# Optimization experiments

Hardware: AMD Instinct MI355X
Metric: run time of the kernel (lower is better)

The kernel has to match this reference:

```python
import jax, jax.numpy as jnp
import numpy as np

B, S, H = 2, 256, 256
R = H  # rdim defaults to hidden_size


def setup_inputs() -> dict:
    key = jax.random.key(0)
    k1, k2, k3 = jax.random.split(key, 3)
    hidden_states = jax.random.normal(k1, (B, S, H), dtype=jnp.float32)
    # Linear weights stored torch-style [out, in]
    Wqkv = jax.random.normal(k2, (3 * R, H), dtype=jnp.float32) * (H ** -0.5)
    bqkv = jnp.zeros((3 * R,), dtype=jnp.float32)
    Wc = jax.random.normal(k3, (R, R), dtype=jnp.float32) * (R ** -0.5)
    bc = jnp.zeros((R,), dtype=jnp.float32)
    return {"hidden_states": hidden_states, "Wqkv": Wqkv, "bqkv": bqkv, "Wc": Wc, "bc": bc}


def reference(hidden_states, Wqkv, bqkv, Wc, bc):
    # qkv projection: [B,S,3R]
    qkv = jnp.einsum('bsh,rh->bsr', hidden_states, Wqkv) + bqkv
    q, k, v = jnp.split(qkv, 3, axis=-1)  # each [B,S,R]
    # Tucker-style outer-product scores: [B,S,L,R]
    scores = jnp.einsum('bsr,blr->bslr', q, k)
    # c_proj mixes the r dimension
    scores = jnp.einsum('bslr,pr->bslp', scores, Wc) + bc
    # rearrange 'b s l r -> (b r) s l' + softmax(dim=-1) == softmax over l axis
    probs = jax.nn.softmax(scores, axis=2)
    # 'brsl,blr->bsr' after rearrange back == 'bslr,blr->bsr'
    return jnp.einsum('bslr,blr->bsr', probs, v)
```

## Files before the change

### kernel.cpp

```cpp
#include <hip/hip_runtime.h>
#include <hip/hip_bf16.h>
#include <math.h>

typedef __bf16 bf16;
typedef _Float16 f16;
typedef __attribute__((ext_vector_type(8))) __bf16 bf16x8;
typedef __attribute__((ext_vector_type(8))) _Float16 f16x8;
typedef __attribute__((ext_vector_type(4))) _Float16 f16x4;
typedef __attribute__((ext_vector_type(4))) float floatx4;

__device__ __forceinline__ void split8(floatx4 a0, floatx4 a1, bf16x8& hi, bf16x8& lo) {
#pragma unroll
    for (int t = 0; t < 4; t++) {
        float v0 = a0[t], v1 = a1[t];
        bf16 h0 = (bf16)v0, h1 = (bf16)v1;
        hi[t] = h0;     lo[t] = (bf16)(v0 - (float)h0);
        hi[t + 4] = h1; lo[t + 4] = (bf16)(v1 - (float)h1);
    }
}

__global__ __launch_bounds__(256, 4)
void proj_kernel(const float* __restrict__ hs, const float* __restrict__ Wq,
                 const float* __restrict__ bq, const float* __restrict__ Wc,
                 f16* __restrict__ q_ws, f16* __restrict__ k_ws,
                 f16* __restrict__ vT_ws, f16* __restrict__ Wc_ws)
{
    const int tid = threadIdx.x;
    if (blockIdx.x >= 384) {
        const int base = (blockIdx.x - 384) * 1024 + tid * 4;
        floatx4 w = *(const floatx4*)(Wc + base);
        f16x4 h;
        h.x = (f16)w.x; h.y = (f16)w.y; h.z = (f16)w.z; h.w = (f16)w.w;
        *(f16x4*)(Wc_ws + base) = h;
        return;
    }
    const int wv = tid >> 6, lane = tid & 63;
    const int quad = lane >> 4, lcol = lane & 15;
    const int wt = blockIdx.x * 4 + wv;
    const int rt = wt / 48, ct = wt - rt * 48;
    const int row0 = rt * 16, col0 = ct * 16;

    const float* arow = hs + (row0 + lcol) * 256;
    const float* brow = Wq + (col0 + lcol) * 256;

    floatx4 acc = {0.f, 0.f, 0.f, 0.f};
#pragma unroll
    for (int ks = 0; ks < 8; ks++) {
        const int h = ks * 32 + quad * 8;
        floatx4 a0 = *(const floatx4*)(arow + h);
        floatx4 a1 = *(const floatx4*)(arow + h + 4);
        floatx4 b0 = *(const floatx4*)(brow + h);
        floatx4 b1 = *(const floatx4*)(brow + h + 4);
        bf16x8 ahi, alo, bhi, blo;
        split8(a0, a1, ahi, alo);
        split8(b0, b1, bhi, blo);
        acc = __builtin_amdgcn_mfma_f32_16x16x32_bf16(ahi, bhi, acc, 0, 0, 0);
        acc = __builtin_amdgcn_mfma_f32_16x16x32_bf16(ahi, blo, acc, 0, 0, 0);
        acc = __builtin_amdgcn_mfma_f32_16x16x32_bf16(alo, bhi, acc, 0, 0, 0);
    }
    const float bias = bq[col0 + lcol];
    const int col = col0 + lcol, seg = col0 >> 8, jj = col & 255;
#pragma unroll
    for (int r = 0; r < 4; r++) {
        const int row = row0 + quad * 4 + r;
        const float val = acc[r] + bias;
        if (seg == 0)      q_ws[row * 256 + jj] = (f16)val;
        else if (seg == 1) k_ws[row * 256 + jj] = (f16)val;
        else               vT_ws[(row >> 8) * 65536 + jj * 256 + (row & 255)] = (f16)val;
    }
}

__global__ __launch_bounds__(512, 2)
void attn_main(const f16* __restrict__ qw, const f16* __restrict__ kw,
               const f16* __restrict__ vT, const f16* __restrict__ Wc16,
               float* __restrict__ out)
{
    __shared__ f16 Wlds[64 * 256];
    __shared__ float obuf[4][4][64];
    __shared__ float sbuf[4][4][64];

    const int bid = blockIdx.x;
    const int pt = bid & 3;
    const int sg = (bid >> 2) & 63;
    const int b  = bid >> 8;
    const int p0 = pt * 64;
    const int tid  = threadIdx.x;
    const int wv   = tid >> 6;
    const int lane = tid & 63;
    const int quad = lane >> 4, lcol = lane & 15;
    const int lq = wv & 3, sh = wv >> 2;
    const int l0w = lq * 64;

    const f16* kbase = kw + b * 65536;
    const f16* vbase = vT + b * 65536;

#pragma unroll
    for (int it = 0; it < 4; it++) {
        const int id = tid + it * 512;
        const int r = id >> 5, c = id & 31;
        const int csrc = c ^ (r & 7);
        uint4 d = *(const uint4*)(Wc16 + (p0 + r) * 256 + csrc * 8);
        *(uint4*)(Wlds + r * 256 + c * 8) = d;
    }
    __syncthreads();

    float osum[2][4], ssum[2][4];

#pragma unroll
    for (int sl = 0; sl < 2; sl++) {
        const int s = sg * 4 + sh * 2 + sl;
        const f16* qrow = qw + (b * 256 + s) * 256;

        floatx4 acc[4][4];
#pragma unroll
        for (int i = 0; i < 4; i++)
#pragma unroll
            for (int j = 0; j < 4; j++)
                acc[i][j] = (floatx4){0.f, 0.f, 0.f, 0.f};

#pragma unroll
        for (int kk = 0; kk < 8; kk++) {
            const int rb = kk * 32 + quad * 8;
            f16x8 qv = *(const f16x8*)(qrow + rb);
            f16x8 kf[4];
#pragma unroll
            for (int i = 0; i < 4; i++)
                kf[i] = *(const f16x8*)(kbase + (l0w + i * 16 + lcol) * 256 + rb);
#pragma unroll
            for (int j = 0; j < 4; j++) {
                f16x8 w8 = *(const f16x8*)(Wlds + (j * 16 + lcol) * 256 +
                                           (((kk * 4 + quad) ^ (lcol & 7)) << 3));
                f16x8 bfr = w8 * qv;
#pragma unroll
                for (int i = 0; i < 4; i++)
                    acc[i][j] = __builtin_amdgcn_mfma_f32_16x16x32_f16(kf[i], bfr, acc[i][j], 0, 0, 0);
            }
        }

        float os[4] = {0.f, 0.f, 0.f, 0.f}, ss[4] = {0.f, 0.f, 0.f, 0.f};
#pragma unroll
        for (int i = 0; i < 4; i++) {
#pragma unroll
            for (int j = 0; j < 4; j++) {
                f16x4 vf = *(const f16x4*)(vbase + (p0 + j * 16 + lcol) * 256 + l0w + i * 16 + quad * 4);
#pragma unroll
                for (int t = 0; t < 4; t++) {
                    const float P = __expf(acc[i][j][t]);
                    os[j] = fmaf(P, (float)vf[t], os[j]);
                    ss[j] += P;
                }
            }
        }
#pragma unroll
        for (int j = 0; j < 4; j++) {
            os[j] += __shfl_xor(os[j], 16);
            os[j] += __shfl_xor(os[j], 32);
            ss[j] += __shfl_xor(ss[j], 16);
            ss[j] += __shfl_xor(ss[j], 32);
            osum[sl][j] = os[j];
            ssum[sl][j] = ss[j];
        }
    }

    if (quad == 0) {
#pragma unroll
        for (int sl = 0; sl < 2; sl++)
#pragma unroll
            for (int j = 0; j < 4; j++) {
                obuf[lq][sh * 2 + sl][j * 16 + lcol] = osum[sl][j];
                sbuf[lq][sh * 2 + sl][j * 16 + lcol] = ssum[sl][j];
            }
    }
    __syncthreads();

    if (tid < 256) {
        const int slot = tid >> 6, p = tid & 63;
        const float O = obuf[0][slot][p] + obuf[1][slot][p] + obuf[2][slot][p] + obuf[3][slot][p];
        const float S = sbuf[0][slot][p] + sbuf[1][slot][p] + sbuf[2][slot][p] + sbuf[3][slot][p];
        out[(b * 256 + sg * 4 + slot) * 256 + p0 + p] = O / S;
    }
}

extern "C" void kernel_launch(void* const* d_in, const int* in_sizes, int n_in,
                              void* d_out, int out_size, void* d_ws, size_t ws_size,
                              hipStream_t stream) {
    const float* hs   = (const float*)d_in[0];
    const float* Wqkv = (const float*)d_in[1];
    const float* bqkv = (const float*)d_in[2];
    const float* Wc   = (const float*)d_in[3];
    float* out = (float*)d_out;

    char* ws = (char*)d_ws;
    f16* q_ws   = (f16*)ws;
    f16* k_ws   = (f16*)(ws + 262144);
    f16* vT_ws  = (f16*)(ws + 524288);
    f16* Wc_ws  = (f16*)(ws + 786432);

    proj_kernel<<<dim3(448), 256, 0, stream>>>(hs, Wqkv, bqkv, Wc, q_ws, k_ws, vT_ws, Wc_ws);
    attn_main<<<dim3(512), 512, 0, stream>>>(q_ws, k_ws, vT_ws, Wc_ws, out);
}
```

Measured before the change: 101.2 us.

## Stage K tiles through LDS with register prefetch, remap waves to seq/l-halves

Each wave now owns one query row and half of a 64-wide l tile. K is staged in 64-row chunks through a swizzled LDS buffer, and the next chunk is prefetched into registers while the current one is consumed. Before, each wave read K fragments straight from global memory, so this shares K across waves through LDS and shrinks the cross-wave reduction to two partials. The cost is extra LDS (32KB more), block-wide barriers in every l-chunk iteration, and a serialized four-step loop.

```diff
diff --git a/kernel.cpp b/kernel.cpp
--- a/kernel.cpp
+++ b/kernel.cpp
@@ -76,8 +76,9 @@
                float* __restrict__ out)
 {
     __shared__ f16 Wlds[64 * 256];
-    __shared__ float obuf[4][4][64];
-    __shared__ float sbuf[4][4][64];
+    __shared__ f16 Klds[64 * 256];
+    __shared__ float obuf[2][4][64];
+    __shared__ float sbuf[2][4][64];
 
     const int bid = blockIdx.x;
     const int pt = bid & 3;
@@ -88,32 +89,52 @@
     const int wv   = tid >> 6;
     const int lane = tid & 63;
     const int quad = lane >> 4, lcol = lane & 15;
-    const int lq = wv & 3, sh = wv >> 2;
-    const int l0w = lq * 64;
+    const int sslot = wv & 3, lh = wv >> 2;
+    const int s = sg * 4 + sslot;
 
     const f16* kbase = kw + b * 65536;
     const f16* vbase = vT + b * 65536;
+    const f16* qrow  = qw + (b * 256 + s) * 256;
 
 #pragma unroll
     for (int it = 0; it < 4; it++) {
-        const int id = tid + it * 512;
+        const int id = it * 512 + tid;
         const int r = id >> 5, c = id & 31;
         const int csrc = c ^ (r & 7);
-        uint4 d = *(const uint4*)(Wc16 + (p0 + r) * 256 + csrc * 8);
-        *(uint4*)(Wlds + r * 256 + c * 8) = d;
-    }
-    __syncthreads();
-
-    float osum[2][4], ssum[2][4];
-
-#pragma unroll
-    for (int sl = 0; sl < 2; sl++) {
-        const int s = sg * 4 + sh * 2 + sl;
-        const f16* qrow = qw + (b * 256 + s) * 256;
-
-        floatx4 acc[4][4];
-#pragma unroll
-        for (int i = 0; i < 4; i++)
+        *(uint4*)(Wlds + r * 256 + c * 8) =
+            *(const uint4*)(Wc16 + (p0 + r) * 256 + csrc * 8);
+    }
+
+    uint4 st[4];
+#pragma unroll
+    for (int it = 0; it < 4; it++) {
+        const int id = it * 512 + tid;
+        const int r = id >> 5, csrc = (id & 31) ^ (r & 7);
+        st[it] = *(const uint4*)(kbase + r * 256 + csrc * 8);
+    }
+
+    float os[4] = {0.f, 0.f, 0.f, 0.f}, ss[4] = {0.f, 0.f, 0.f, 0.f};
+
+    for (int lq = 0; lq < 4; lq++) {
+#pragma unroll
+        for (int it = 0; it < 4; it++) {
+            const int id = it * 512 + tid;
+            const int r = id >> 5, c = id & 31;
+            *(uint4*)(Klds + r * 256 + c * 8) = st[it];
+        }
+        if (lq < 3) {
+#pragma unroll
+            for (int it = 0; it < 4; it++) {
+                const int id = it * 512 + tid;
+                const int r = id >> 5, csrc = (id & 31) ^ (r & 7);
+                st[it] = *(const uint4*)(kbase + ((lq + 1) * 64 + r) * 256 + csrc * 8);
+            }
+        }
+        __syncthreads();
+
+        floatx4 acc[2][4];
+#pragma unroll
+        for (int i = 0; i < 2; i++)
 #pragma unroll
             for (int j = 0; j < 4; j++)
                 acc[i][j] = (floatx4){0.f, 0.f, 0.f, 0.f};
@@ -122,27 +143,24 @@
         for (int kk = 0; kk < 8; kk++) {
             const int rb = kk * 32 + quad * 8;
             f16x8 qv = *(const f16x8*)(qrow + rb);
-            f16x8 kf[4];
-#pragma unroll
-            for (int i = 0; i < 4; i++)
-                kf[i] = *(const f16x8*)(kbase + (l0w + i * 16 + lcol) * 256 + rb);
+            const int sw = ((kk * 4 + quad) ^ (lcol & 7)) << 3;
+            f16x8 kf0 = *(const f16x8*)(Klds + (lh * 32 + lcol) * 256 + sw);
+            f16x8 kf1 = *(const f16x8*)(Klds + (lh * 32 + 16 + lcol) * 256 + sw);
 #pragma unroll
             for (int j = 0; j < 4; j++) {
-                f16x8 w8 = *(const f16x8*)(Wlds + (j * 16 + lcol) * 256 +
-                                           (((kk * 4 + quad) ^ (lcol & 7)) << 3));
+                f16x8 w8 = *(const f16x8*)(Wlds + (j * 16 + lcol) * 256 + sw);
                 f16x8 bfr = w8 * qv;
-#pragma unroll
-                for (int i = 0; i < 4; i++)
-                    acc[i][j] = __builtin_amdgcn_mfma_f32_16x16x32_f16(kf[i], bfr, acc[i][j], 0, 0, 0);
+                acc[0][j] = __builtin_amdgcn_mfma_f32_16x16x32_f16(kf0, bfr, acc[0][j], 0, 0, 0);
+                acc[1][j] = __builtin_amdgcn_mfma_f32_16x16x32_f16(kf1, bfr, acc[1][j], 0, 0, 0);
             }
         }
 
-        float os[4] = {0.f, 0.f, 0.f, 0.f}, ss[4] = {0.f, 0.f, 0.f, 0.f};
-#pragma unroll
-        for (int i = 0; i < 4; i++) {
+        const int lbase = lq * 64 + lh * 32;
+#pragma unroll
+        for (int i = 0; i < 2; i++) {
 #pragma unroll
             for (int j = 0; j < 4; j++) {
-                f16x4 vf = *(const f16x4*)(vbase + (p0 + j * 16 + lcol) * 256 + l0w + i * 16 + quad * 4);
+                f16x4 vf = *(const f16x4*)(vbase + (p0 + j * 16 + lcol) * 256 + lbase + i * 16 + quad * 4);
 #pragma unroll
                 for (int t = 0; t < 4; t++) {
                     const float P = __expf(acc[i][j][t]);
@@ -151,32 +169,29 @@
                 }
             }
         }
+        if (lq < 3) __syncthreads();
+    }
+
+#pragma unroll
+    for (int j = 0; j < 4; j++) {
+        os[j] += __shfl_xor(os[j], 16);
+        os[j] += __shfl_xor(os[j], 32);
+        ss[j] += __shfl_xor(ss[j], 16);
+        ss[j] += __shfl_xor(ss[j], 32);
+    }
+    if (quad == 0) {
 #pragma unroll
         for (int j = 0; j < 4; j++) {
-            os[j] += __shfl_xor(os[j], 16);
-            os[j] += __shfl_xor(os[j], 32);
-            ss[j] += __shfl_xor(ss[j], 16);
-            ss[j] += __shfl_xor(ss[j], 32);
-            osum[sl][j] = os[j];
-            ssum[sl][j] = ss[j];
-        }
-    }
-
-    if (quad == 0) {
-#pragma unroll
-        for (int sl = 0; sl < 2; sl++)
-#pragma unroll
-            for (int j = 0; j < 4; j++) {
-                obuf[lq][sh * 2 + sl][j * 16 + lcol] = osum[sl][j];
-                sbuf[lq][sh * 2 + sl][j * 16 + lcol] = ssum[sl][j];
-            }
+            obuf[lh][sslot][j * 16 + lcol] = os[j];
+            sbuf[lh][sslot][j * 16 + lcol] = ss[j];
+        }
     }
     __syncthreads();
 
     if (tid < 256) {
         const int slot = tid >> 6, p = tid & 63;
-        const float O = obuf[0][slot][p] + obuf[1][slot][p] + obuf[2][slot][p] + obuf[3][slot][p];
-        const float S = sbuf[0][slot][p] + sbuf[1][slot][p] + sbuf[2][slot][p] + sbuf[3][slot][p];
+        const float O = obuf[0][slot][p] + obuf[1][slot][p];
+        const float S = sbuf[0][slot][p] + sbuf[1][slot][p];
         out[(b * 256 + sg * 4 + slot) * 256 + p0 + p] = O / S;
     }
 }
```

New measurement: 113.1 us. 11.7% more time.

## Split L across 8 waves and process two s rows per block

Applied to the files above, without the earlier changes.

Each block now handles 2 sequence rows instead of 4, with all 8 waves splitting the L dimension into 32-wide slices. Each wave handles both s rows, so each K fragment and Wc LDS read feeds two q rows. The grid doubles to 1024 blocks. This costs twice as many Wc tile loads into LDS across the grid and an 8-way cross-wave reduction, in exchange for better fragment reuse and more parallelism.

```diff
diff --git a/kernel.cpp b/kernel.cpp
--- a/kernel.cpp
+++ b/kernel.cpp
@@ -76,108 +76,116 @@
                float* __restrict__ out)
 {
     __shared__ f16 Wlds[64 * 256];
-    __shared__ float obuf[4][4][64];
-    __shared__ float sbuf[4][4][64];
+    __shared__ float obuf[8][2][64];
+    __shared__ float sbuf[8][2][64];
 
     const int bid = blockIdx.x;
     const int pt = bid & 3;
-    const int sg = (bid >> 2) & 63;
-    const int b  = bid >> 8;
+    const int sg = (bid >> 2) & 127;
+    const int b  = bid >> 9;
     const int p0 = pt * 64;
     const int tid  = threadIdx.x;
     const int wv   = tid >> 6;
     const int lane = tid & 63;
     const int quad = lane >> 4, lcol = lane & 15;
-    const int lq = wv & 3, sh = wv >> 2;
-    const int l0w = lq * 64;
+    const int l0w = wv * 32;
 
     const f16* kbase = kw + b * 65536;
     const f16* vbase = vT + b * 65536;
+    const f16* qrow0 = qw + (b * 256 + sg * 2) * 256;
+    const f16* qrow1 = qrow0 + 256;
 
 #pragma unroll
     for (int it = 0; it < 4; it++) {
-        const int id = tid + it * 512;
+        const int id = it * 512 + tid;
         const int r = id >> 5, c = id & 31;
         const int csrc = c ^ (r & 7);
-        uint4 d = *(const uint4*)(Wc16 + (p0 + r) * 256 + csrc * 8);
-        *(uint4*)(Wlds + r * 256 + c * 8) = d;
+        *(uint4*)(Wlds + r * 256 + c * 8) =
+            *(const uint4*)(Wc16 + (p0 + r) * 256 + csrc * 8);
     }
     __syncthreads();
 
-    float osum[2][4], ssum[2][4];
-
-#pragma unroll
-    for (int sl = 0; sl < 2; sl++) {
-        const int s = sg * 4 + sh * 2 + sl;
-        const f16* qrow = qw + (b * 256 + s) * 256;
-
-        floatx4 acc[4][4];
-#pragma unroll
-        for (int i = 0; i < 4; i++)
+    floatx4 acc[2][2][4];
+#pragma unroll
+    for (int s = 0; s < 2; s++)
+#pragma unroll
+        for (int i = 0; i < 2; i++)
 #pragma unroll
             for (int j = 0; j < 4; j++)
-                acc[i][j] = (floatx4){0.f, 0.f, 0.f, 0.f};
-
-#pragma unroll
-        for (int kk = 0; kk < 8; kk++) {
-            const int rb = kk * 32 + quad * 8;
-            f16x8 qv = *(const f16x8*)(qrow + rb);
-            f16x8 kf[4];
-#pragma unroll
-            for (int i = 0; i < 4; i++)
-                kf[i] = *(const f16x8*)(kbase + (l0w + i * 16 + lcol) * 256 + rb);
+                acc[s][i][j] = (floatx4){0.f, 0.f, 0.f, 0.f};
+
+#pragma unroll
+    for (int kk = 0; kk < 8; kk++) {
+        const int rb = kk * 32 + quad * 8;
+        f16x8 qv0 = *(const f16x8*)(qrow0 + rb);
+        f16x8 qv1 = *(const f16x8*)(qrow1 + rb);
+        f16x8 kf0 = *(const f16x8*)(kbase + (l0w + lcol) * 256 + rb);
+        f16x8 kf1 = *(const f16x8*)(kbase + (l0w + 16 + lcol) * 256 + rb);
+        const int sw = ((kk * 4 + quad) ^ (lcol & 7)) << 3;
+#pragma unroll
+        for (int j = 0; j < 4; j++) {
+            f16x8 w8 = *(const f16x8*)(Wlds + (j * 16 + lcol) * 256 + sw);
+            f16x8 bf0 = w8 * qv0;
+            f16x8 bf1 = w8 * qv1;
+            acc[0][0][j] = __builtin_amdgcn_mfma_f32_16x16x32_f16(kf0, bf0, acc[0][0][j], 0, 0, 0);
+            acc[0][1][j] = __builtin_amdgcn_mfma_f32_16x16x32_f16(kf1, bf0, acc[0][1][j], 0, 0, 0);
+            acc[1][0][j] = __builtin_amdgcn_mfma_f32_16x16x32_f16(kf0, bf1, acc[1][0][j], 0, 0, 0);
+            acc[1][1][j] = __builtin_amdgcn_mfma_f32_16x16x32_f16(kf1, bf1, acc[1][1][j], 0, 0, 0);
+        }
+    }
+
+    float os[2][4] = {{0.f,0.f,0.f,0.f},{0.f,0.f,0.f,0.f}};
+    float ss[2][4] = {{0.f,0.f,0.f,0.f},{0.f,0.f,0.f,0.f}};
+#pragma unroll
+    for (int i = 0; i < 2; i++) {
+#pragma unroll
+        for (int j = 0; j < 4; j++) {
+            f16x4 vf = *(const f16x4*)(vbase + (p0 + j * 16 + lcol) * 256 + l0w + i * 16 + quad * 4);
+            float vF0 = (float)vf[0], vF1 = (float)vf[1], vF2 = (float)vf[2], vF3 = (float)vf[3];
+#pragma unroll
+            for (int s = 0; s < 2; s++) {
+                const float P0 = __expf(acc[s][i][j][0]);
+                const float P1 = __expf(acc[s][i][j][1]);
+                const float P2 = __expf(acc[s][i][j][2]);
+                const float P3 = __expf(acc[s][i][j][3]);
+                os[s][j] = fmaf(P0, vF0, os[s][j]);
+                os[s][j] = fmaf(P1, vF1, os[s][j]);
+                os[s][j] = fmaf(P2, vF2, os[s][j]);
+                os[s][j] = fmaf(P3, vF3, os[s][j]);
+                ss[s][j] += (P0 + P1) + (P2 + P3);
+            }
+        }
+    }
+
+#pragma unroll
+    for (int s = 0; s < 2; s++)
+#pragma unroll
+        for (int j = 0; j < 4; j++) {
+            os[s][j] += __shfl_xor(os[s][j], 16);
+            os[s][j] += __shfl_xor(os[s][j], 32);
+            ss[s][j] += __shfl_xor(ss[s][j], 16);
+            ss[s][j] += __shfl_xor(ss[s][j], 32);
+        }
+    if (quad == 0) {
+#pragma unroll
+        for (int s = 0; s < 2; s++)
 #pragma unroll
             for (int j = 0; j < 4; j++) {
-                f16x8 w8 = *(const f16x8*)(Wlds + (j * 16 + lcol) * 256 +
-                                           (((kk * 4 + quad) ^ (lcol & 7)) << 3));
-                f16x8 bfr = w8 * qv;
-#pragma unroll
-                for (int i = 0; i < 4; i++)
-                    acc[i][j] = __builtin_amdgcn_mfma_f32_16x16x32_f16(kf[i], bfr, acc[i][j], 0, 0, 0);
+                obuf[wv][s][j * 16 + lcol] = os[s][j];
+                sbuf[wv][s][j * 16 + lcol] = ss[s][j];
             }
-        }
-
-        float os[4] = {0.f, 0.f, 0.f, 0.f}, ss[4] = {0.f, 0.f, 0.f, 0.f};
-#pragma unroll
-        for (int i = 0; i < 4; i++) {
-#pragma unroll
-            for (int j = 0; j < 4; j++) {
-                f16x4 vf = *(const f16x4*)(vbase + (p0 + j * 16 + lcol) * 256 + l0w + i * 16 + quad * 4);
-#pragma unroll
-                for (int t = 0; t < 4; t++) {
-                    const float P = __expf(acc[i][j][t]);
-                    os[j] = fmaf(P, (float)vf[t], os[j]);
-                    ss[j] += P;
-                }
-            }
-        }
-#pragma unroll
-        for (int j = 0; j < 4; j++) {
-            os[j] += __shfl_xor(os[j], 16);
-            os[j] += __shfl_xor(os[j], 32);
-            ss[j] += __shfl_xor(ss[j], 16);
-            ss[j] += __shfl_xor(ss[j], 32);
-            osum[sl][j] = os[j];
-            ssum[sl][j] = ss[j];
-        }
-    }
-
-    if (quad == 0) {
-#pragma unroll
-        for (int sl = 0; sl < 2; sl++)
-#pragma unroll
-            for (int j = 0; j < 4; j++) {
-                obuf[lq][sh * 2 + sl][j * 16 + lcol] = osum[sl][j];
-                sbuf[lq][sh * 2 + sl][j * 16 + lcol] = ssum[sl][j];
-            }
     }
     __syncthreads();
 
-    if (tid < 256) {
-        const int slot = tid >> 6, p = tid & 63;
-        const float O = obuf[0][slot][p] + obuf[1][slot][p] + obuf[2][slot][p] + obuf[3][slot][p];
-        const float S = sbuf[0][slot][p] + sbuf[1][slot][p] + sbuf[2][slot][p] + sbuf[3][slot][p];
-        out[(b * 256 + sg * 4 + slot) * 256 + p0 + p] = O / S;
+    if (tid < 128) {
+        const int si = tid >> 6, p = tid & 63;
+        float O = 0.f, S = 0.f;
+#pragma unroll
+        for (int w = 0; w < 8; w++) {
+            O += obuf[w][si][p];
+            S += sbuf[w][si][p];
+        }
+        out[(b * 256 + sg * 2 + si) * 256 + p0 + p] = O / S;
     }
 }
 
@@ -197,5 +205,5 @@
     f16* Wc_ws  = (f16*)(ws + 786432);
 
     proj_kernel<<<dim3(448), 256, 0, stream>>>(hs, Wqkv, bqkv, Wc, q_ws, k_ws, vT_ws, Wc_ws);
-    attn_main<<<dim3(512), 512, 0, stream>>>(q_ws, k_ws, vT_ws, Wc_ws, out);
-}
+    attn_main<<<dim3(1024), 512, 0, stream>>>(q_ws, k_ws, vT_ws, Wc_ws, out);
+}
```

Measured after the change: 101.6 us. Within noise of the previous version (+0.4%).

## Split attention over key blocks, stage K and V tiles in LDS, merge partials

Applied to the files above, without the earlier changes.

Each attention block now handles one 64-key slice for eight query rows, with every wave owning one query row. The K tile, Wc tile and V^T tile are staged into LDS, so the MFMA loop and the softmax-weighted V sum read from shared memory rather than global memory. Per-slice numerators and denominators go to a workspace, and a new merge kernel sums the four slices and divides. This adds a third launch and about 4 MB of partial-sum traffic, and LDS use grows to roughly 73 KB per block, which may limit occupancy.

```diff
diff --git a/kernel.cpp b/kernel.cpp
--- a/kernel.cpp
+++ b/kernel.cpp
@@ -71,114 +71,128 @@
 }
 
 __global__ __launch_bounds__(512, 2)
-void attn_main(const f16* __restrict__ qw, const f16* __restrict__ kw,
-               const f16* __restrict__ vT, const f16* __restrict__ Wc16,
-               float* __restrict__ out)
+void attn_partial(const f16* __restrict__ qw, const f16* __restrict__ kw,
+                  const f16* __restrict__ vT, const f16* __restrict__ Wc16,
+                  float* __restrict__ osum_ws, float* __restrict__ ssum_ws)
 {
+    __shared__ f16 Klds[64 * 256];
     __shared__ f16 Wlds[64 * 256];
-    __shared__ float obuf[4][4][64];
-    __shared__ float sbuf[4][4][64];
+    __shared__ f16 vTlds[64 * 68];
 
     const int bid = blockIdx.x;
     const int pt = bid & 3;
-    const int sg = (bid >> 2) & 63;
-    const int b  = bid >> 8;
+    const int lq = (bid >> 2) & 3;
+    const int sg = (bid >> 4) & 31;
+    const int b  = bid >> 9;
     const int p0 = pt * 64;
+    const int l0 = lq * 64;
     const int tid  = threadIdx.x;
     const int wv   = tid >> 6;
     const int lane = tid & 63;
     const int quad = lane >> 4, lcol = lane & 15;
-    const int lq = wv & 3, sh = wv >> 2;
-    const int l0w = lq * 64;
+    const int s = sg * 8 + wv;
 
     const f16* kbase = kw + b * 65536;
     const f16* vbase = vT + b * 65536;
+    const f16* qrow  = qw + (b * 256 + s) * 256;
 
 #pragma unroll
     for (int it = 0; it < 4; it++) {
-        const int id = tid + it * 512;
+        const int id = it * 512 + tid;
         const int r = id >> 5, c = id & 31;
         const int csrc = c ^ (r & 7);
-        uint4 d = *(const uint4*)(Wc16 + (p0 + r) * 256 + csrc * 8);
-        *(uint4*)(Wlds + r * 256 + c * 8) = d;
+        *(uint4*)(Klds + r * 256 + c * 8) =
+            *(const uint4*)(kbase + (l0 + r) * 256 + csrc * 8);
+    }
+#pragma unroll
+    for (int it = 0; it < 4; it++) {
+        const int id = it * 512 + tid;
+        const int r = id >> 5, c = id & 31;
+        const int csrc = c ^ (r & 7);
+        *(uint4*)(Wlds + r * 256 + c * 8) =
+            *(const uint4*)(Wc16 + (p0 + r) * 256 + csrc * 8);
+    }
+#pragma unroll
+    for (int it = 0; it < 2; it++) {
+        const int id = it * 512 + tid;
+        const int p = id >> 4, c = id & 15;
+        *(f16x4*)(vTlds + p * 68 + c * 4) =
+            *(const f16x4*)(vbase + (p0 + p) * 256 + l0 + c * 4);
     }
     __syncthreads();
 
-    float osum[2][4], ssum[2][4];
-
-#pragma unroll
-    for (int sl = 0; sl < 2; sl++) {
-        const int s = sg * 4 + sh * 2 + sl;
-        const f16* qrow = qw + (b * 256 + s) * 256;
-
-        floatx4 acc[4][4];
+    floatx4 acc[4][4];
+#pragma unroll
+    for (int i = 0; i < 4; i++)
+#pragma unroll
+        for (int j = 0; j < 4; j++)
+            acc[i][j] = (floatx4){0.f, 0.f, 0.f, 0.f};
+
+#pragma unroll
+    for (int kk = 0; kk < 8; kk++) {
+        const int rb = kk * 32 + quad * 8;
+        f16x8 qv = *(const f16x8*)(qrow + rb);
+        const int sw = ((kk * 4 + quad) ^ (lcol & 7)) << 3;
+        f16x8 kf[4];
 #pragma unroll
         for (int i = 0; i < 4; i++)
-#pragma unroll
-            for (int j = 0; j < 4; j++)
-                acc[i][j] = (floatx4){0.f, 0.f, 0.f, 0.f};
-
-#pragma unroll
-        for (int kk = 0; kk < 8; kk++) {
-            const int rb = kk * 32 + quad * 8;
-            f16x8 qv = *(const f16x8*)(qrow + rb);
-            f16x8 kf[4];
+            kf[i] = *(const f16x8*)(Klds + (i * 16 + lcol) * 256 + sw);
+#pragma unroll
+        for (int j = 0; j < 4; j++) {
+            f16x8 w8 = *(const f16x8*)(Wlds + (j * 16 + lcol) * 256 + sw);
+            f16x8 bfr = w8 * qv;
 #pragma unroll
             for (int i = 0; i < 4; i++)
-                kf[i] = *(const f16x8*)(kbase + (l0w + i * 16 + lcol) * 256 + rb);
-#pragma unroll
-            for (int j = 0; j < 4; j++) {
-                f16x8 w8 = *(const f16x8*)(Wlds + (j * 16 + lcol) * 256 +
-                                           (((kk * 4 + quad) ^ (lcol & 7)) << 3));
-                f16x8 bfr = w8 * qv;
-#pragma unroll
-                for (int i = 0; i < 4; i++)
-                    acc[i][j] = __builtin_amdgcn_mfma_f32_16x16x32_f16(kf[i], bfr, acc[i][j], 0, 0, 0);
+                acc[i][j] = __builtin_amdgcn_mfma_f32_16x16x32_f16(kf[i], bfr, acc[i][j], 0, 0, 0);
+        }
+    }
+
+    float os[4] = {0.f, 0.f, 0.f, 0.f}, ss[4] = {0.f, 0.f, 0.f, 0.f};
+#pragma unroll
+    for (int i = 0; i < 4; i++) {
+#pragma unroll
+        for (int j = 0; j < 4; j++) {
+            f16x4 vf = *(const f16x4*)(vTlds + (j * 16 + lcol) * 68 + i * 16 + quad * 4);
+#pragma unroll
+            for (int t = 0; t < 4; t++) {
+                const float P = __expf(acc[i][j][t]);
+                os[j] = fmaf(P, (float)vf[t], os[j]);
+                ss[j] += P;
             }
         }
-
-        float os[4] = {0.f, 0.f, 0.f, 0.f}, ss[4] = {0.f, 0.f, 0.f, 0.f};
-#pragma unroll
-        for (int i = 0; i < 4; i++) {
-#pragma unroll
-            for (int j = 0; j < 4; j++) {
-                f16x4 vf = *(const f16x4*)(vbase + (p0 + j * 16 + lcol) * 256 + l0w + i * 16 + quad * 4);
-#pragma unroll
-                for (int t = 0; t < 4; t++) {
-                    const float P = __expf(acc[i][j][t]);
-                    os[j] = fmaf(P, (float)vf[t], os[j]);
-                    ss[j] += P;
-                }
-            }
+    }
+
+#pragma unroll
+    for (int j = 0; j < 4; j++) {
+        os[j] += __shfl_xor(os[j], 16);
+        os[j] += __shfl_xor(os[j], 32);
+        ss[j] += __shfl_xor(ss[j], 16);
+        ss[j] += __shfl_xor(ss[j], 32);
+    }
+    if (quad == 0) {
+        const int base = ((b * 256 + s) * 4 + lq) * 256 + p0;
+#pragma unroll
+        for (int j = 0; j < 4; j++) {
+            osum_ws[base + j * 16 + lcol] = os[j];
+            ssum_ws[base + j * 16 + lcol] = ss[j];
         }
-#pragma unroll
-        for (int j = 0; j < 4; j++) {
-            os[j] += __shfl_xor(os[j], 16);
-            os[j] += __shfl_xor(os[j], 32);
-            ss[j] += __shfl_xor(ss[j], 16);
-            ss[j] += __shfl_xor(ss[j], 32);
-            osum[sl][j] = os[j];
-            ssum[sl][j] = ss[j];
-        }
-    }
-
-    if (quad == 0) {
-#pragma unroll
-        for (int sl = 0; sl < 2; sl++)
-#pragma unroll
-            for (int j = 0; j < 4; j++) {
-                obuf[lq][sh * 2 + sl][j * 16 + lcol] = osum[sl][j];
-                sbuf[lq][sh * 2 + sl][j * 16 + lcol] = ssum[sl][j];
-            }
-    }
-    __syncthreads();
-
-    if (tid < 256) {
-        const int slot = tid >> 6, p = tid & 63;
-        const float O = obuf[0][slot][p] + obuf[1][slot][p] + obuf[2][slot][p] + obuf[3][slot][p];
-        const float S = sbuf[0][slot][p] + sbuf[1][slot][p] + sbuf[2][slot][p] + sbuf[3][slot][p];
-        out[(b * 256 + sg * 4 + slot) * 256 + p0 + p] = O / S;
-    }
+    }
+}
+
+__global__ __launch_bounds__(256, 4)
+void merge_kernel(const float* __restrict__ osum_ws, const float* __restrict__ ssum_ws,
+                  float* __restrict__ out)
+{
+    const int g = blockIdx.x * 256 + threadIdx.x;
+    const int p = g & 255, bs = g >> 8;
+    const int base = bs * 1024 + p;
+    float O = 0.f, S = 0.f;
+#pragma unroll
+    for (int lq = 0; lq < 4; lq++) {
+        O += osum_ws[base + lq * 256];
+        S += ssum_ws[base + lq * 256];
+    }
+    out[g] = O / S;
 }
 
 extern "C" void kernel_launch(void* const* d_in, const int* in_sizes, int n_in,
@@ -195,7 +209,10 @@
     f16* k_ws   = (f16*)(ws + 262144);
     f16* vT_ws  = (f16*)(ws + 524288);
     f16* Wc_ws  = (f16*)(ws + 786432);
+    float* osum_ws = (float*)(ws + 1048576);
+    float* ssum_ws = (float*)(ws + 3145728);
 
     proj_kernel<<<dim3(448), 256, 0, stream>>>(hs, Wqkv, bqkv, Wc, q_ws, k_ws, vT_ws, Wc_ws);
-    attn_main<<<dim3(512), 512, 0, stream>>>(q_ws, k_ws, vT_ws, Wc_ws, out);
-}
+    attn_partial<<<dim3(1024), 512, 0, stream>>>(q_ws, k_ws, vT_ws, Wc_ws, osum_ws, ssum_ws);
+    merge_kernel<<<dim3(512), 256, 0, stream>>>(osum_ws, ssum_ws, out);
+}
```

After: 90.28 us. -10.8%, faster.
